# Performance work log

Measured on AMD Instinct MI355X. Metric: run time of the kernel, lower is better.

The kernel has to match this reference:

```python
import jax, jax.numpy as jnp
import numpy as np

E = 512      # embed_dim
H = 8        # num_heads
HD = E // H  # head_dim
TGT = 512
SRC = 2048
B = 16


def setup_inputs() -> dict:
    key = jax.random.key(0)
    ks = jax.random.split(key, 10)
    inp = {
        "query": jax.random.normal(ks[0], (TGT, B, E), dtype=jnp.float32),
        "key": jax.random.normal(ks[1], (SRC, B, E), dtype=jnp.float32),
        "value": jax.random.normal(ks[2], (SRC, B, E), dtype=jnp.float32),
        "in_proj_weight": jax.random.normal(ks[3], (3 * E, E), dtype=jnp.float32) * 0.02,
        "in_proj_bias": jax.random.normal(ks[4], (3 * E,), dtype=jnp.float32) * 0.02,
        "bias_k": jax.random.normal(ks[5], (1, 1, E), dtype=jnp.float32) * 0.02,
        "bias_v": jax.random.normal(ks[6], (1, 1, E), dtype=jnp.float32) * 0.02,
        "out_proj_weight": jax.random.normal(ks[7], (E, E), dtype=jnp.float32) * 0.02,
        "out_proj_bias": jnp.zeros((E,), dtype=jnp.float32),
        "key_padding_mask": jax.random.randint(ks[8], (B, SRC), 0, 2).astype(bool),
    }
    return inp


def reference(query, key, value, in_proj_weight, in_proj_bias, bias_k, bias_v,
              out_proj_weight, out_proj_bias, key_padding_mask):
    tgt_len, bsz, embed_dim = query.shape
    scaling = float(HD) ** -0.5

    # manual in-projection (query != key, key is value -> separate q, fused kv)
    q = query @ in_proj_weight[:E].T + in_proj_bias[:E]
    k = key @ in_proj_weight[E:2 * E].T + in_proj_bias[E:2 * E]
    v = value @ in_proj_weight[2 * E:].T + in_proj_bias[2 * E:]
    q = q * scaling

    # bias_k / bias_v concatenation along src dim; pad key_padding_mask with False
    k = jnp.concatenate([k, jnp.broadcast_to(bias_k, (1, bsz, E))], axis=0)
    v = jnp.concatenate([v, jnp.broadcast_to(bias_v, (1, bsz, E))], axis=0)
    kpm = jnp.pad(key_padding_mask, ((0, 0), (0, 1)))  # [B, SRC+1]

    src_len = k.shape[0]
    # [len, B, E] -> [B*H, len, HD]
    q = q.reshape(tgt_len, bsz * H, HD).transpose(1, 0, 2)
    k = k.reshape(src_len, bsz * H, HD).transpose(1, 0, 2)
    v = v.reshape(src_len, bsz * H, HD).transpose(1, 0, 2)

    scores = jnp.einsum('bth,bsh->bts', q, k)  # [B*H, TGT, SRC+1]
    mask = kpm[:, None, None, :]               # [B, 1, 1, SRC+1]
    scores = scores.reshape(bsz, H, tgt_len, src_len)
    scores = jnp.where(mask, -jnp.inf, scores).reshape(bsz * H, tgt_len, src_len)
    attn = jax.nn.softmax(scores, axis=-1)

    out = jnp.einsum('bts,bsh->bth', attn, v)                 # [B*H, TGT, HD]
    out = out.transpose(1, 0, 2).reshape(tgt_len, bsz, E)     # [TGT, B, E]
    out = out @ out_proj_weight.T + out_proj_bias
    return out, attn
```

## Files before the change

kernel.cpp:

```cpp
#include <hip/hip_runtime.h>
#include <hip/hip_bf16.h>

#define E    512
#define H    8
#define HD   64
#define TGT  512
#define SRC  2048
#define S1   2049
#define S1P  2112
#define NB   16
#define BH   128
#define NCH  33
#define PW   2120

typedef __attribute__((ext_vector_type(8))) short short8;
typedef __attribute__((ext_vector_type(4))) float floatx4;

__device__ __forceinline__ unsigned short f2bf(float x) {
    unsigned u = __float_as_uint(x);
    u = (u + 0x7FFF + ((u >> 16) & 1)) >> 16;
    return (unsigned short)u;
}

__device__ __forceinline__ unsigned short f2bf1(float x) {
    __hip_bfloat16 h = __float2bfloat16(x);
    return *(unsigned short*)&h;
}

__device__ __forceinline__ int4 cvt8(const float4 f0, const float4 f1) {
    __hip_bfloat162 o[4];
    o[0] = __float22bfloat162_rn({f0.x, f0.y});
    o[1] = __float22bfloat162_rn({f0.z, f0.w});
    o[2] = __float22bfloat162_rn({f1.x, f1.y});
    o[3] = __float22bfloat162_rn({f1.z, f1.w});
    return *(int4*)o;
}

__global__ __launch_bounds__(256) void cvt_bf16(const float* __restrict__ src,
    unsigned short* __restrict__ dst, const int n8)
{
    const int i = blockIdx.x * 256 + threadIdx.x;
    if (i >= n8) return;
    const float4 f0 = ((const float4*)src)[(size_t)i * 2];
    const float4 f1 = ((const float4*)src)[(size_t)i * 2 + 1];
    ((int4*)dst)[i] = cvt8(f0, f1);
}

__global__ __launch_bounds__(256) void proj_gemm(const unsigned short* __restrict__ X,
    const unsigned short* __restrict__ W, const float* __restrict__ bias,
    unsigned short* __restrict__ Y, const int ld, const float scale)
{
    __shared__ __align__(16) unsigned short As[128][72];
    __shared__ __align__(16) unsigned short Bs[64][72];
    const int tid  = threadIdx.x;
    const int c0   = blockIdx.x << 6;
    const int r0   = blockIdx.y << 7;
    const int w    = tid >> 6, lane = tid & 63, c = lane & 15, quad = lane >> 4;
    floatx4 acc[2][4] = {};
    for (int k0 = 0; k0 < E; k0 += 64) {
#pragma unroll
        for (int i = 0; i < 4; ++i) {
            const int idx = tid + (i << 8);
            const int r = idx >> 3, q = (idx & 7) << 3;
            *(int4*)&As[r][q] = *(const int4*)&X[(size_t)(r0 + r) * E + k0 + q];
        }
#pragma unroll
        for (int i = 0; i < 2; ++i) {
            const int idx = tid + (i << 8);
            const int r = idx >> 3, q = (idx & 7) << 3;
            *(int4*)&Bs[r][q] = *(const int4*)&W[(size_t)(c0 + r) * E + k0 + q];
        }
        __syncthreads();
#pragma unroll
        for (int kh = 0; kh < 2; ++kh) {
            short8 a0 = *(const short8*)&As[(w << 5) + c][(kh << 5) + (quad << 3)];
            short8 a1 = *(const short8*)&As[(w << 5) + 16 + c][(kh << 5) + (quad << 3)];
#pragma unroll
            for (int n = 0; n < 4; ++n) {
                short8 b = *(const short8*)&Bs[(n << 4) + c][(kh << 5) + (quad << 3)];
                acc[0][n] = __builtin_amdgcn_mfma_f32_16x16x32_bf16(a0, b, acc[0][n], 0, 0, 0);
                acc[1][n] = __builtin_amdgcn_mfma_f32_16x16x32_bf16(a1, b, acc[1][n], 0, 0, 0);
            }
        }
        __syncthreads();
    }
#pragma unroll
    for (int mt = 0; mt < 2; ++mt) {
#pragma unroll
        for (int reg = 0; reg < 4; ++reg) {
            const int rg = r0 + (w << 5) + (mt << 4) + (quad << 2) + reg;
            const int t = rg >> 4, b = rg & 15;
#pragma unroll
            for (int n = 0; n < 4; ++n) {
                const int col = c0 + (n << 4) + c;
                const int h = col >> 6, hd = col & 63;
                const float v = (acc[mt][n][reg] + bias[col]) * scale;
                Y[((size_t)(b * H + h) * ld + t) * HD + hd] = f2bf1(v);
            }
        }
    }
}

#define FB_BIAS  8192
#define FB_KPAD  64512
#define FB_VPAD  516096
__global__ __launch_bounds__(256) void fill_bias(const float* __restrict__ bk,
    const float* __restrict__ bv,
    unsigned short* __restrict__ kbuf, unsigned short* __restrict__ vtbuf)
{
    const int idx = blockIdx.x * 256 + threadIdx.x;
    if (idx < FB_BIAS) {
        const int bh = idx >> 6, hd = idx & 63, h = bh & 7;
        kbuf[((size_t)bh * S1P + SRC) * HD + hd] = f2bf(bk[h * HD + hd]);
        vtbuf[((size_t)bh * HD + hd) * S1P + SRC] = f2bf(bv[h * HD + hd]);
    } else if (idx < FB_BIAS + FB_KPAD) {
        const int i = idx - FB_BIAS;
        const int bh = i / 504, o = i % 504;
        const int4 z = {0, 0, 0, 0};
        ((int4*)&kbuf[((size_t)bh * S1P + S1) * HD])[o] = z;
    } else if (idx < FB_BIAS + FB_KPAD + FB_VPAD) {
        const int i = idx - FB_BIAS - FB_KPAD;
        const int bh = i / 4032, r = i % 4032;
        const int hd = r / 63, s = S1 + r % 63;
        vtbuf[((size_t)bh * HD + hd) * S1P + s] = 0;
    }
}

__global__ __launch_bounds__(256) void transpose_v(const unsigned short* __restrict__ vbuf,
    unsigned short* __restrict__ vtbuf)
{
    __shared__ __align__(16) unsigned short T[64][72];
    const int tid = threadIdx.x;
    const int s0  = blockIdx.x << 6;
    const int bh  = blockIdx.y;
#pragma unroll
    for (int i = 0; i < 2; ++i) {
        const int idx = tid + (i << 8);
        const int s = idx >> 3, q = (idx & 7) << 3;
        *(int4*)&T[s][q] = *(const int4*)&vbuf[((size_t)bh * SRC + s0 + s) * HD + q];
    }
    __syncthreads();
#pragma unroll
    for (int i = 0; i < 2; ++i) {
        const int idx = tid + (i << 8);
        const int hd = idx >> 3, sq = (idx & 7) << 3;
        unsigned short tmp[8];
#pragma unroll
        for (int j = 0; j < 8; ++j) tmp[j] = T[sq + j][hd];
        *(int4*)&vtbuf[((size_t)bh * HD + hd) * S1P + s0 + sq] = *(int4*)tmp;
    }
}

__global__ __launch_bounds__(512, 4) void attn_fused(
    const unsigned short* __restrict__ qbh,
    const unsigned short* __restrict__ kbuf,
    const unsigned short* __restrict__ vtbuf,
    const int* __restrict__ kpm,
    float* __restrict__ attn, unsigned short* __restrict__ ctx)
{
    __shared__ __align__(16) unsigned short P[16][PW];
    __shared__ float cpart[16][68];
    __shared__ float sums[8][16];
    __shared__ float linv[16];
    const int tid = threadIdx.x;
    const int t0  = blockIdx.x << 4;
    const int bh  = blockIdx.y;
    const int bb  = bh >> 3;
    const int w = tid >> 6, lane = tid & 63, c = lane & 15, quad = lane >> 4;

    const unsigned short* qr = &qbh[((size_t)bh * TGT + t0 + c) * HD + (quad << 3)];
    short8 qa0 = *(const short8*)qr;
    short8 qa1 = *(const short8*)(qr + 32);

#define LOADK(D0, D1, M, CH) do {                                               \
        const unsigned short* kb_ = &kbuf[((size_t)bh * S1P + ((CH) << 6)) * HD]; \
        _Pragma("unroll")                                                       \
        for (int n_ = 0; n_ < 4; ++n_) {                                        \
            const unsigned short* kr_ = kb_ + ((n_ << 4) + c) * HD + (quad << 3); \
            D0[n_] = *(const short8*)kr_;                                       \
            D1[n_] = *(const short8*)(kr_ + 32);                                \
        }                                                                       \
        _Pragma("unroll")                                                       \
        for (int n_ = 0; n_ < 4; ++n_) {                                        \
            const int s_ = ((CH) << 6) + (n_ << 4) + c;                         \
            M[n_] = (s_ < SRC) ? (kpm[bb * SRC + s_] ? 3e38f : 0.f)             \
                               : ((s_ == SRC) ? 0.f : 3e38f);                   \
        }                                                                       \
    } while (0)

#define PIN(D0, D1) asm volatile("" :                                          \
        "+v"(D0[0]), "+v"(D0[1]), "+v"(D0[2]), "+v"(D0[3]),                     \
        "+v"(D1[0]), "+v"(D1[1]), "+v"(D1[2]), "+v"(D1[3]))

#define QK_COMPUTE(CH, B0, B1, M) do {                                          \
        const int s0_ = (CH) << 6;                                              \
        floatx4 sc_[4] = {};                                                    \
        _Pragma("unroll")                                                       \
        for (int n_ = 0; n_ < 4; ++n_) {                                        \
            sc_[n_] = __builtin_amdgcn_mfma_f32_16x16x32_bf16(qa0, B0[n_], sc_[n_], 0, 0, 0); \
            sc_[n_] = __builtin_amdgcn_mfma_f32_16x16x32_bf16(qa1, B1[n_], sc_[n_], 0, 0, 0); \
        }                                                                       \
        _Pragma("unroll")                                                       \
        for (int n_ = 0; n_ < 4; ++n_) {                                        \
            _Pragma("unroll")                                                   \
            for (int rg_ = 0; rg_ < 4; ++rg_) {                                 \
                const float p_ = __expf(sc_[n_][rg_] - M[n_]);                  \
                rs[rg_] += p_;                                                  \
                P[(quad << 2) + rg_][s0_ + (n_ << 4) + c] = f2bf1(p_);          \
            }                                                                   \
        }                                                                       \
    } while (0)

    float rs[4] = {0.f, 0.f, 0.f, 0.f};
    short8 kb0[4], kb1[4];
    float mk[4];
    LOADK(kb0, kb1, mk, w);
    int ch;
    for (ch = w; ch + 8 < NCH; ch += 8) {
        short8 nb0[4], nb1[4];
        float nm[4];
        LOADK(nb0, nb1, nm, ch + 8);
        PIN(nb0, nb1);
        QK_COMPUTE(ch, kb0, kb1, mk);
#pragma unroll
        for (int n = 0; n < 4; ++n) { kb0[n] = nb0[n]; kb1[n] = nb1[n]; mk[n] = nm[n]; }
    }
    QK_COMPUTE(ch, kb0, kb1, mk);

#pragma unroll
    for (int reg = 0; reg < 4; ++reg) {
        float v = rs[reg];
        v += __shfl_xor(v, 1); v += __shfl_xor(v, 2);
        v += __shfl_xor(v, 4); v += __shfl_xor(v, 8);
        rs[reg] = v;
    }
    if (c == 0) {
#pragma unroll
        for (int reg = 0; reg < 4; ++reg)
            sums[w][(quad << 2) + reg] = rs[reg];
    }
    __syncthreads();
    if (tid < 16) {
        float s = 0.f;
#pragma unroll
        for (int i = 0; i < 8; ++i) s += sums[i][tid];
        linv[tid] = 1.0f / s;
    }
    __syncthreads();

    const int hs = w & 3, kh2 = w >> 2;
    const int base = kh2 * 1056;
    const unsigned short* vrow = &vtbuf[((size_t)bh * HD + (hs << 4) + c) * S1P + base];
#define LV(U) (*(const short8*)&vrow[((U) << 5) + (quad << 3)])
#define LP(U) (*(const short8*)&P[c][base + ((U) << 5) + (quad << 3)])
    floatx4 ca0 = {}, ca1 = {};
    short8 vt = LV(32);
    short8 v0 = LV(0), v1 = LV(1), v2 = LV(2), v3 = LV(3);
#pragma unroll
    for (int u = 0; u < 32; u += 4) {
        ca0 = __builtin_amdgcn_mfma_f32_16x16x32_bf16(LP(u),     v0, ca0, 0, 0, 0);
        ca1 = __builtin_amdgcn_mfma_f32_16x16x32_bf16(LP(u + 1), v1, ca1, 0, 0, 0);
        if (u < 28) { v0 = LV(u + 4); v1 = LV(u + 5); }
        ca0 = __builtin_amdgcn_mfma_f32_16x16x32_bf16(LP(u + 2), v2, ca0, 0, 0, 0);
        ca1 = __builtin_amdgcn_mfma_f32_16x16x32_bf16(LP(u + 3), v3, ca1, 0, 0, 0);
        if (u < 28) { v2 = LV(u + 6); v3 = LV(u + 7); }
    }
    ca0 = __builtin_amdgcn_mfma_f32_16x16x32_bf16(LP(32), vt, ca0, 0, 0, 0);
    if (kh2 == 1) {
#pragma unroll
        for (int reg = 0; reg < 4; ++reg)
            cpart[(quad << 2) + reg][(hs << 4) + c] = ca0[reg] + ca1[reg];
    }
    __syncthreads();
    if (kh2 == 0) {
#pragma unroll
        for (int reg = 0; reg < 4; ++reg) {
            const int row = (quad << 2) + reg;
            const float v = (ca0[reg] + ca1[reg] + cpart[row][(hs << 4) + c]) * linv[row];
            ctx[((size_t)bh * TGT + t0 + row) * HD + (hs << 4) + c] = f2bf1(v);
        }
    }

    for (int p = w; p < 16; p += 8) {
        const int s0 = p << 7;
#pragma unroll
        for (int r = 0; r < 16; ++r) {
            const unsigned pk = *(const unsigned*)&P[r][s0 + (lane << 1)];
            const float li = linv[r];
            const size_t a = ((size_t)bh * TGT + t0 + r) * S1 + s0 + (lane << 1);
            attn[a]     = __uint_as_float((pk & 0xFFFFu) << 16) * li;
            attn[a + 1] = __uint_as_float(pk & 0xFFFF0000u) * li;
        }
    }
    if (w == 7 && lane < 16) {
        const float p = __uint_as_float((unsigned)P[lane][2048] << 16) * linv[lane];
        attn[((size_t)bh * TGT + t0 + lane) * S1 + 2048] = p;
    }
#undef LOADK
#undef PIN
#undef QK_COMPUTE
#undef LV
#undef LP
}

__global__ __launch_bounds__(256) void outproj_gemm(const unsigned short* __restrict__ ctx,
    const unsigned short* __restrict__ W, const float* __restrict__ bias,
    float* __restrict__ out)
{
    __shared__ __align__(16) unsigned short As[128][72];
    __shared__ __align__(16) unsigned short Bs[64][72];
    const int tid = threadIdx.x;
    const int c0  = blockIdx.x << 6;
    const int r0  = blockIdx.y << 7;
    const int w   = tid >> 6, lane = tid & 63, c = lane & 15, quad = lane >> 4;
    floatx4 acc[2][4] = {};
    for (int k0 = 0; k0 < E; k0 += 64) {
        const int h = k0 >> 6;
#pragma unroll
        for (int i = 0; i < 4; ++i) {
            const int idx = tid + (i << 8);
            const int r = idx >> 3, q = (idx & 7) << 3;
            const int rg = r0 + r, t = rg >> 4, b = rg & 15;
            *(int4*)&As[r][q] = *(const int4*)&ctx[((size_t)(b * H + h) * TGT + t) * HD + q];
        }
#pragma unroll
        for (int i = 0; i < 2; ++i) {
            const int idx = tid + (i << 8);
            const int r = idx >> 3, q = (idx & 7) << 3;
            *(int4*)&Bs[r][q] = *(const int4*)&W[(size_t)(c0 + r) * E + k0 + q];
        }
        __syncthreads();
#pragma unroll
        for (int kh = 0; kh < 2; ++kh) {
            short8 a0 = *(const short8*)&As[(w << 5) + c][(kh << 5) + (quad << 3)];
            short8 a1 = *(const short8*)&As[(w << 5) + 16 + c][(kh << 5) + (quad << 3)];
#pragma unroll
            for (int n = 0; n < 4; ++n) {
                short8 b = *(const short8*)&Bs[(n << 4) + c][(kh << 5) + (quad << 3)];
                acc[0][n] = __builtin_amdgcn_mfma_f32_16x16x32_bf16(a0, b, acc[0][n], 0, 0, 0);
                acc[1][n] = __builtin_amdgcn_mfma_f32_16x16x32_bf16(a1, b, acc[1][n], 0, 0, 0);
            }
        }
        __syncthreads();
    }
#pragma unroll
    for (int mt = 0; mt < 2; ++mt) {
#pragma unroll
        for (int reg = 0; reg < 4; ++reg) {
            const int rg = r0 + (w << 5) + (mt << 4) + (quad << 2) + reg;
#pragma unroll
            for (int n = 0; n < 4; ++n) {
                const int col = c0 + (n << 4) + c;
                out[(size_t)rg * E + col] = acc[mt][n][reg] + bias[col];
            }
        }
    }
}

extern "C" void kernel_launch(void* const* d_in, const int* in_sizes, int n_in,
                              void* d_out, int out_size, void* d_ws, size_t ws_size,
                              hipStream_t stream)
{
    const float* query  = (const float*)d_in[0];
    const float* key    = (const float*)d_in[1];
    const float* value  = (const float*)d_in[2];
    const float* ipw    = (const float*)d_in[3];
    const float* ipb    = (const float*)d_in[4];
    const float* bias_k = (const float*)d_in[5];
    const float* bias_v = (const float*)d_in[6];
    const float* opw    = (const float*)d_in[7];
    const float* opb    = (const float*)d_in[8];
    const int*   kpm    = (const int*)d_in[9];

    float* out  = (float*)d_out;
    float* attn = out + (size_t)TGT * NB * E;

    unsigned short* k_bf = (unsigned short*)attn;
    unsigned short* v_bf = k_bf + (size_t)16777216;
    unsigned short* vbuf = v_bf + (size_t)16777216;

    char* ws = (char*)d_ws;
    unsigned short* q_bf  = (unsigned short*)ws;
    unsigned short* wi_bf = q_bf  + (size_t)4194304;
    unsigned short* wo_bf = wi_bf + (size_t)786432;
    unsigned short* qbh   = wo_bf + (size_t)262144;
    unsigned short* kbuf  = qbh   + (size_t)4194304;
    unsigned short* vtbuf = kbuf  + (size_t)17301504;
    unsigned short* ctx   = vtbuf + (size_t)17301504;

    cvt_bf16<<<dim3(2048), 256, 0, stream>>>(query, q_bf, 524288);
    cvt_bf16<<<dim3(8192), 256, 0, stream>>>(key,   k_bf, 2097152);
    cvt_bf16<<<dim3(8192), 256, 0, stream>>>(value, v_bf, 2097152);
    cvt_bf16<<<dim3(384),  256, 0, stream>>>(ipw,   wi_bf, 98304);
    cvt_bf16<<<dim3(128),  256, 0, stream>>>(opw,   wo_bf, 32768);

    proj_gemm<<<dim3(8, 64),  256, 0, stream>>>(q_bf, wi_bf,          ipb,         qbh,  TGT, 0.125f);
    proj_gemm<<<dim3(8, 256), 256, 0, stream>>>(k_bf, wi_bf + 262144, ipb + E,     kbuf, S1P, 1.0f);
    proj_gemm<<<dim3(8, 256), 256, 0, stream>>>(v_bf, wi_bf + 524288, ipb + 2 * E, vbuf, SRC, 1.0f);

    fill_bias<<<dim3(2300), 256, 0, stream>>>(bias_k, bias_v, kbuf, vtbuf);
    transpose_v<<<dim3(32, 128), 256, 0, stream>>>(vbuf, vtbuf);

    attn_fused<<<dim3(32, 128), 512, 0, stream>>>(qbh, kbuf, vtbuf, kpm, attn, ctx);
    outproj_gemm<<<dim3(8, 64), 256, 0, stream>>>(ctx, wo_bf, opb, out);
}
```

Before: 1.075 ms.

## Merge Q/K/V projections into one launch and fuse V transpose into epilogue

Replaces the three projection GEMM launches with a single 3D-grid kernel that picks Q, K or V by blockIdx.z; Q blocks beyond row 64 exit early. For V, the epilogue stages the tile in shared memory and writes it transposed straight into vtbuf. This removes the separate transpose kernel and the round trip through the intermediate V buffer. The cost is some wasted early-exit blocks and strided shared-memory reads in the V epilogue.

Result: faster. 1.025 ms (-4.7%).

```diff
diff --git a/kernel.cpp b/kernel.cpp
--- a/kernel.cpp
+++ b/kernel.cpp
@@ -46,12 +46,20 @@
     ((int4*)dst)[i] = cvt8(f0, f1);
 }
 
-__global__ __launch_bounds__(256) void proj_gemm(const unsigned short* __restrict__ X,
-    const unsigned short* __restrict__ W, const float* __restrict__ bias,
-    unsigned short* __restrict__ Y, const int ld, const float scale)
-{
+__global__ __launch_bounds__(256) void proj_all(
+    const unsigned short* __restrict__ q_bf, const unsigned short* __restrict__ k_bf,
+    const unsigned short* __restrict__ v_bf, const unsigned short* __restrict__ wi,
+    const float* __restrict__ ipb,
+    unsigned short* __restrict__ qbh, unsigned short* __restrict__ kbuf,
+    unsigned short* __restrict__ vtbuf)
+{
+    const int z = blockIdx.z;
+    if (z == 0 && blockIdx.y >= 64) return;
     __shared__ __align__(16) unsigned short As[128][72];
     __shared__ __align__(16) unsigned short Bs[64][72];
+    const unsigned short* X = (z == 0) ? q_bf : (z == 1) ? k_bf : v_bf;
+    const unsigned short* W = wi + (size_t)z * 262144;
+    const float* bias = ipb + z * E;
     const int tid  = threadIdx.x;
     const int c0   = blockIdx.x << 6;
     const int r0   = blockIdx.y << 7;
@@ -84,6 +92,36 @@
         }
         __syncthreads();
     }
+    if (z == 2) {
+        const int h = c0 >> 6;
+#pragma unroll
+        for (int mt = 0; mt < 2; ++mt) {
+#pragma unroll
+            for (int reg = 0; reg < 4; ++reg) {
+                const int local = (w << 5) + (mt << 4) + (quad << 2) + reg;
+#pragma unroll
+                for (int n = 0; n < 4; ++n) {
+                    const int hd = (n << 4) + c;
+                    As[local][hd] = f2bf1(acc[mt][n][reg] + bias[c0 + hd]);
+                }
+            }
+        }
+        __syncthreads();
+        const int s0v = blockIdx.y << 3;
+#pragma unroll
+        for (int i = 0; i < 4; ++i) {
+            const int idx = tid + (i << 8);
+            const int b = idx & 15, hd = idx >> 4;
+            unsigned short tmp[8];
+#pragma unroll
+            for (int j = 0; j < 8; ++j) tmp[j] = As[(j << 4) + b][hd];
+            *(int4*)&vtbuf[((size_t)(b * H + h) * HD + hd) * S1P + s0v] = *(int4*)tmp;
+        }
+        return;
+    }
+    unsigned short* Y = (z == 0) ? qbh : kbuf;
+    const int ld = (z == 0) ? TGT : S1P;
+    const float scale = (z == 0) ? 0.125f : 1.0f;
 #pragma unroll
     for (int mt = 0; mt < 2; ++mt) {
 #pragma unroll
@@ -123,31 +161,6 @@
         const int bh = i / 4032, r = i % 4032;
         const int hd = r / 63, s = S1 + r % 63;
         vtbuf[((size_t)bh * HD + hd) * S1P + s] = 0;
-    }
-}
-
-__global__ __launch_bounds__(256) void transpose_v(const unsigned short* __restrict__ vbuf,
-    unsigned short* __restrict__ vtbuf)
-{
-    __shared__ __align__(16) unsigned short T[64][72];
-    const int tid = threadIdx.x;
-    const int s0  = blockIdx.x << 6;
-    const int bh  = blockIdx.y;
-#pragma unroll
-    for (int i = 0; i < 2; ++i) {
-        const int idx = tid + (i << 8);
-        const int s = idx >> 3, q = (idx & 7) << 3;
-        *(int4*)&T[s][q] = *(const int4*)&vbuf[((size_t)bh * SRC + s0 + s) * HD + q];
-    }
-    __syncthreads();
-#pragma unroll
-    for (int i = 0; i < 2; ++i) {
-        const int idx = tid + (i << 8);
-        const int hd = idx >> 3, sq = (idx & 7) << 3;
-        unsigned short tmp[8];
-#pragma unroll
-        for (int j = 0; j < 8; ++j) tmp[j] = T[sq + j][hd];
-        *(int4*)&vtbuf[((size_t)bh * HD + hd) * S1P + s0 + sq] = *(int4*)tmp;
     }
 }
 
@@ -377,7 +390,6 @@
 
     unsigned short* k_bf = (unsigned short*)attn;
     unsigned short* v_bf = k_bf + (size_t)16777216;
-    unsigned short* vbuf = v_bf + (size_t)16777216;
 
     char* ws = (char*)d_ws;
     unsigned short* q_bf  = (unsigned short*)ws;
@@ -394,12 +406,10 @@
     cvt_bf16<<<dim3(384),  256, 0, stream>>>(ipw,   wi_bf, 98304);
     cvt_bf16<<<dim3(128),  256, 0, stream>>>(opw,   wo_bf, 32768);
 
-    proj_gemm<<<dim3(8, 64),  256, 0, stream>>>(q_bf, wi_bf,          ipb,         qbh,  TGT, 0.125f);
-    proj_gemm<<<dim3(8, 256), 256, 0, stream>>>(k_bf, wi_bf + 262144, ipb + E,     kbuf, S1P, 1.0f);
-    proj_gemm<<<dim3(8, 256), 256, 0, stream>>>(v_bf, wi_bf + 524288, ipb + 2 * E, vbuf, SRC, 1.0f);
+    proj_all<<<dim3(8, 256, 3), 256, 0, stream>>>(q_bf, k_bf, v_bf, wi_bf, ipb,
+                                                  qbh, kbuf, vtbuf);
 
     fill_bias<<<dim3(2300), 256, 0, stream>>>(bias_k, bias_v, kbuf, vtbuf);
-    transpose_v<<<dim3(32, 128), 256, 0, stream>>>(vbuf, vtbuf);
 
     attn_fused<<<dim3(32, 128), 512, 0, stream>>>(qbh, kbuf, vtbuf, kpm, attn, ctx);
     outproj_gemm<<<dim3(8, 64), 256, 0, stream>>>(ctx, wo_bf, opb, out);
```
